# Performance work log

Measured on AMD Instinct MI355X. Metric: run time of the kernel, lower is better.

Reference implementation:

```python
import jax, jax.numpy as jnp
import numpy as np

T, B, D, H = 2048, 2, 1024, 16
NH, DH = H // 2, D // H   # 8 heads per direction, d_head = 64
DFF = 4096


def layer_norm(x, g, b, eps=1e-5):
    mu = jnp.mean(x, axis=-1, keepdims=True)
    var = jnp.mean(jnp.square(x - mu), axis=-1, keepdims=True)
    return (x - mu) * jax.lax.rsqrt(var + eps) * g + b


def rel_shift(x):
    # x: [q, k, b, n] -> Transformer-XL relative shift
    q, k, b, n = x.shape
    x = jnp.concatenate([jnp.zeros((q, 1, b, n), x.dtype), x], axis=1)
    return x.reshape(k + 1, q, b, n)[1:].reshape(q, k, b, n)


def rel_attn(w, r, mask, qkv_w, r_w, r_w_bias, r_r_bias):
    # w: [T, B, D], r: [R, 1, D], mask: [T, T] bool (True = masked)
    t, b, _ = w.shape
    heads = jnp.einsum('tbd,ed->tbe', w, qkv_w)              # [T,B,3*NH*DH]
    q, k, v = jnp.split(heads, 3, axis=-1)
    q = q.reshape(t, b, NH, DH)
    k = k.reshape(t, b, NH, DH)
    v = v.reshape(t, b, NH, DH)
    rk = jnp.einsum('rd,ed->re', r[:, 0, :], r_w).reshape(-1, NH, DH)  # [R,NH,DH]
    AC = jnp.einsum('ibnd,jbnd->ijbn', q + r_w_bias, k)
    BD = rel_shift(jnp.einsum('ibnd,jnd->ijbn', q + r_r_bias, rk))
    score = (AC + BD) * (1.0 / np.sqrt(DH))
    score = jnp.where(mask[:, :, None, None], jnp.finfo(score.dtype).min, score)
    prob = jax.nn.softmax(score, axis=1)
    vec = jnp.einsum('ijbn,jbnd->ibnd', prob, v)
    return vec.reshape(t, b, NH * DH)


def setup_inputs() -> dict:
    key = jax.random.key(0)
    ks = jax.random.split(key, 24)
    s = 0.02
    causal = jnp.triu(jnp.ones((T, T), dtype=bool), k=1)
    return {
        'x': jax.random.normal(ks[0], (T, B, D), jnp.float32),
        'pos': jax.random.normal(ks[1], (T, 1, D), jnp.float32),
        'mask_fwd': causal,
        'mask_bwd': causal,
        'ln1_g': jnp.ones((D,), jnp.float32), 'ln1_b': jnp.zeros((D,), jnp.float32),
        'ln2_g': jnp.ones((D,), jnp.float32), 'ln2_b': jnp.zeros((D,), jnp.float32),
        'ln3_g': jnp.ones((D,), jnp.float32), 'ln3_b': jnp.zeros((D,), jnp.float32),
        'qkv_f': jax.random.normal(ks[2], (3 * NH * DH, D), jnp.float32) * s,
        'rnet_f': jax.random.normal(ks[3], (NH * DH, D), jnp.float32) * s,
        'rwb_f': jax.random.normal(ks[4], (NH, DH), jnp.float32) * s,
        'rrb_f': jax.random.normal(ks[5], (NH, DH), jnp.float32) * s,
        'qkv_b': jax.random.normal(ks[6], (3 * NH * DH, D), jnp.float32) * s,
        'rnet_b': jax.random.normal(ks[7], (NH * DH, D), jnp.float32) * s,
        'rwb_b': jax.random.normal(ks[8], (NH, DH), jnp.float32) * s,
        'rrb_b': jax.random.normal(ks[9], (NH, DH), jnp.float32) * s,
        'wo': jax.random.normal(ks[10], (D, D), jnp.float32) * s,
        'bo': jnp.zeros((D,), jnp.float32),
        'w1': jax.random.normal(ks[11], (DFF, D), jnp.float32) * s,
        'b1': jnp.zeros((DFF,), jnp.float32),
        'w2': jax.random.normal(ks[12], (D, DFF), jnp.float32) * s,
        'b2': jnp.zeros((D,), jnp.float32),
    }


def reference(x, pos, mask_fwd, mask_bwd,
              ln1_g, ln1_b, ln2_g, ln2_b, ln3_g, ln3_b,
              qkv_f, rnet_f, rwb_f, rrb_f,
              qkv_b, rnet_b, rwb_b, rrb_b,
              wo, bo, w1, b1, w2, b2):
    # --- bidirectional relative attention ---
    q_fwd = layer_norm(x, ln1_g, ln1_b)
    q_bwd = layer_norm(jnp.flip(x, axis=0), ln2_g, ln2_b)
    out_fwd = rel_attn(q_fwd, pos, mask_fwd, qkv_f, rnet_f, rwb_f, rrb_f)
    out_bwd = rel_attn(q_bwd, pos, mask_bwd, qkv_b, rnet_b, rwb_b, rrb_b)
    out = jnp.concatenate([out_fwd, jnp.flip(out_bwd, axis=0)], axis=-1)
    out = jnp.einsum('tbd,ed->tbe', out, wo) + bo
    h = x + out                     # postprocess_attn: dropout(id) + residual
    # --- feed forward: LN -> Linear -> ReLU -> Linear -> residual ---
    y = layer_norm(h, ln3_g, ln3_b)
    y = jax.nn.relu(jnp.einsum('tbd,fd->tbf', y, w1) + b1)
    y = jnp.einsum('tbf,df->tbd', y, w2) + b2
    return h + y
```

## Files before the change

kernel.cpp:

```cpp
#include <hip/hip_runtime.h>
#include <cstdint>
#include <cstddef>


typedef unsigned short ushort_t;
typedef __bf16 bf16x8 __attribute__((ext_vector_type(8)));
typedef float f32x4 __attribute__((ext_vector_type(4)));
typedef unsigned short us8 __attribute__((ext_vector_type(8)));
typedef unsigned short us4 __attribute__((ext_vector_type(4)));

#define DEV static __device__ __forceinline__

DEV ushort_t f2bf(float x) {
  union { float f; unsigned u; } v; v.f = x;
  unsigned r = (v.u + 0x7FFFu + ((v.u >> 16) & 1u)) >> 16;
  return (ushort_t)r;
}
DEV ushort_t f2bt(float x) {
  union { float f; unsigned u; } v; v.f = x;
  return (ushort_t)(v.u >> 16);
}
DEV float bf2f(ushort_t h) {
  union { unsigned u; float f; } v; v.u = ((unsigned)h) << 16;
  return v.f;
}
DEV float fexp2(float x) { float r; asm("v_exp_f32 %0, %1" : "=v"(r) : "v"(x)); return r; }
DEV f32x4 mfma16(bf16x8 a, bf16x8 b, f32x4 c) {
  return __builtin_amdgcn_mfma_f32_16x16x32_bf16(a, b, c, 0, 0, 0);
}
DEV void gld16(const void* g, void* l) {
  __builtin_amdgcn_global_load_lds((const __attribute__((address_space(1))) void*)g,
                                   (__attribute__((address_space(3))) void*)l,
                                   16, 0, 0);
}

constexpr float SCLQ = 0.125f * 1.44269504088896f;

constexpr size_t O_QKV_F  = 0;
constexpr size_t O_QKV_B  = 3145728;
constexpr size_t O_RNET_F = 6291456;
constexpr size_t O_RNET_B = 7340032;
constexpr size_t O_WO     = 8388608;
constexpr size_t O_W1     = 10485760;
constexpr size_t O_W2     = 18874368;
constexpr size_t O_RKREV_F= 27262976;
constexpr size_t O_RKREV_B= 29360128;
constexpr size_t O_QAC_F  = 31457280;
constexpr size_t O_QBD_F  = 35651584;
constexpr size_t O_KK_F   = 39845888;
constexpr size_t O_VT_F   = 44040192;
constexpr size_t O_QAC_B  = 48234496;
constexpr size_t O_QBD_B  = 52428800;
constexpr size_t O_KK_B   = 56623104;
constexpr size_t O_VT_B   = 60817408;
constexpr size_t O_H      = 65011712;
constexpr size_t O_LN3    = 81788928;
constexpr size_t ZONE     = 90177536;
constexpr size_t O_POS    = ZONE + 0;
constexpr size_t O_LN1    = ZONE + 4194304;
constexpr size_t O_LN2    = ZONE + 12582912;
constexpr size_t O_HEADS_F= ZONE + 20971520;
constexpr size_t O_HEADS_B= ZONE + 33554432;
constexpr size_t O_ACAT   = ZONE + 0;
constexpr size_t O_FFNM   = ZONE + 8388608;

struct CvtArgs {
  const float* src[8];
  ushort_t* dst[8];
  int bstart[8];
};
__global__ __launch_bounds__(256)
void cvt_all_k(CvtArgs a) {
  int bx = blockIdx.x;
  int s = 0;
#pragma unroll
  for (int k = 1; k < 8; ++k) if (bx >= a.bstart[k]) s = k;
  int i = (bx - a.bstart[s]) * 256 + threadIdx.x;
  float4 v = reinterpret_cast<const float4*>(a.src[s])[i];
  us4 o; o[0] = f2bf(v.x); o[1] = f2bf(v.y); o[2] = f2bf(v.z); o[3] = f2bf(v.w);
  reinterpret_cast<us4*>(a.dst[s])[i] = o;
}

__global__ __launch_bounds__(256)
void ln_dual_k(const float* __restrict__ x,
               const float* __restrict__ g1, const float* __restrict__ b1,
               const float* __restrict__ g2, const float* __restrict__ b2,
               ushort_t* __restrict__ o1, ushort_t* __restrict__ o2) {
  __shared__ float sbuf[8];
  const int row = blockIdx.x;
  const int tid = threadIdx.x;
  const float* xr = x + (size_t)row * 1024;
  float4 v = reinterpret_cast<const float4*>(xr)[tid];
  float s  = v.x + v.y + v.z + v.w;
  float s2 = v.x*v.x + v.y*v.y + v.z*v.z + v.w*v.w;
  for (int m = 32; m >= 1; m >>= 1) { s += __shfl_xor(s, m, 64); s2 += __shfl_xor(s2, m, 64); }
  int w = tid >> 6;
  if ((tid & 63) == 0) { sbuf[w] = s; sbuf[4 + w] = s2; }
  __syncthreads();
  float S  = sbuf[0] + sbuf[1] + sbuf[2] + sbuf[3];
  float S2 = sbuf[4] + sbuf[5] + sbuf[6] + sbuf[7];
  float mu  = S * (1.f / 1024.f);
  float var = S2 * (1.f / 1024.f) - mu * mu;
  float inv = rsqrtf(var + 1e-5f);
  int t = row >> 1, b = row & 1;
  size_t r2 = ((size_t)(2047 - t) * 2 + b) * 1024;
  float4 G1 = reinterpret_cast<const float4*>(g1)[tid];
  float4 B1 = reinterpret_cast<const float4*>(b1)[tid];
  float4 G2 = reinterpret_cast<const float4*>(g2)[tid];
  float4 B2 = reinterpret_cast<const float4*>(b2)[tid];
  float n0 = (v.x - mu) * inv, n1 = (v.y - mu) * inv, n2 = (v.z - mu) * inv, n3 = (v.w - mu) * inv;
  us4 a, c;
  a[0] = f2bf(n0 * G1.x + B1.x); a[1] = f2bf(n1 * G1.y + B1.y);
  a[2] = f2bf(n2 * G1.z + B1.z); a[3] = f2bf(n3 * G1.w + B1.w);
  c[0] = f2bf(n0 * G2.x + B2.x); c[1] = f2bf(n1 * G2.y + B2.y);
  c[2] = f2bf(n2 * G2.z + B2.z); c[3] = f2bf(n3 * G2.w + B2.w);
  reinterpret_cast<us4*>(o1 + (size_t)row * 1024)[tid] = a;
  reinterpret_cast<us4*>(o2 + r2)[tid] = c;
}

__global__ __launch_bounds__(256)
void ln_one_k(const float* __restrict__ x,
              const float* __restrict__ g1, const float* __restrict__ b1,
              ushort_t* __restrict__ o1) {
  __shared__ float sbuf[8];
  const int row = blockIdx.x;
  const int tid = threadIdx.x;
  const float* xr = x + (size_t)row * 1024;
  float4 v = reinterpret_cast<const float4*>(xr)[tid];
  float s  = v.x + v.y + v.z + v.w;
  float s2 = v.x*v.x + v.y*v.y + v.z*v.z + v.w*v.w;
  for (int m = 32; m >= 1; m >>= 1) { s += __shfl_xor(s, m, 64); s2 += __shfl_xor(s2, m, 64); }
  int w = tid >> 6;
  if ((tid & 63) == 0) { sbuf[w] = s; sbuf[4 + w] = s2; }
  __syncthreads();
  float S  = sbuf[0] + sbuf[1] + sbuf[2] + sbuf[3];
  float S2 = sbuf[4] + sbuf[5] + sbuf[6] + sbuf[7];
  float mu  = S * (1.f / 1024.f);
  float var = S2 * (1.f / 1024.f) - mu * mu;
  float inv = rsqrtf(var + 1e-5f);
  float4 G1 = reinterpret_cast<const float4*>(g1)[tid];
  float4 B1 = reinterpret_cast<const float4*>(b1)[tid];
  us4 a;
  a[0] = f2bf((v.x - mu) * inv * G1.x + B1.x);
  a[1] = f2bf((v.y - mu) * inv * G1.y + B1.y);
  a[2] = f2bf((v.z - mu) * inv * G1.z + B1.z);
  a[3] = f2bf((v.w - mu) * inv * G1.w + B1.w);
  reinterpret_cast<us4*>(o1 + (size_t)row * 1024)[tid] = a;
}

template <int EPI>
__global__ __launch_bounds__(256)
void gemm_bt(const ushort_t* __restrict__ A, const ushort_t* __restrict__ B,
             void* __restrict__ C, const float* __restrict__ bias,
             const float* __restrict__ resid, int M, int N, int K) {
  __shared__ ushort_t As[128 * 64];
  __shared__ ushort_t Bs[128 * 64];
  const int tid = threadIdx.x;
  const int lane = tid & 63;
  const int w = tid >> 6;
  const int wm = w >> 1, wn = w & 1;
  const int row0 = blockIdx.y * 128, col0 = blockIdx.x * 128;
  const int lr = lane & 15;
  const int lkb = (lane >> 4) * 8;
  const int rr = lane >> 3;
  const int scb = ((lane & 7) ^ rr) * 8;
  const f32x4 fz = {0.f, 0.f, 0.f, 0.f};
  f32x4 acc[4][4];
#pragma unroll
  for (int i = 0; i < 4; ++i)
#pragma unroll
    for (int j = 0; j < 4; ++j) acc[i][j] = fz;

  for (int k0 = 0; k0 < K; k0 += 64) {
    __syncthreads();
#pragma unroll
    for (int it = 0; it < 4; ++it) {
      int rbase = it * 32 + w * 8;
      gld16(A + (size_t)(row0 + rbase + rr) * K + k0 + scb, (char*)As + rbase * 128);
      gld16(B + (size_t)(col0 + rbase + rr) * K + k0 + scb, (char*)Bs + rbase * 128);
    }
    __syncthreads();
#pragma unroll
    for (int kk = 0; kk < 64; kk += 32) {
      bf16x8 af[4], bfr[4];
#pragma unroll
      for (int mi = 0; mi < 4; ++mi) {
        int r = wm * 64 + mi * 16 + lr;
        int off = (r * 128 + (kk + lkb) * 2) ^ ((r & 7) << 4);
        af[mi] = *reinterpret_cast<const bf16x8*>((char*)As + off);
      }
#pragma unroll
      for (int ni = 0; ni < 4; ++ni) {
        int r = wn * 64 + ni * 16 + lr;
        int off = (r * 128 + (kk + lkb) * 2) ^ ((r & 7) << 4);
        bfr[ni] = *reinterpret_cast<const bf16x8*>((char*)Bs + off);
      }
#pragma unroll
      for (int mi = 0; mi < 4; ++mi)
#pragma unroll
        for (int ni = 0; ni < 4; ++ni)
          acc[mi][ni] = mfma16(af[mi], bfr[ni], acc[mi][ni]);
    }
  }
#pragma unroll
  for (int mi = 0; mi < 4; ++mi)
#pragma unroll
    for (int ni = 0; ni < 4; ++ni)
#pragma unroll
      for (int r = 0; r < 4; ++r) {
        int row = row0 + wm * 64 + mi * 16 + (lane >> 4) * 4 + r;
        int col = col0 + wn * 64 + ni * 16 + lr;
        float v = acc[mi][ni][r];
        if (EPI == 0) {
          ((ushort_t*)C)[(size_t)row * N + col] = f2bf(v);
        } else if (EPI == 1) {
          v += bias[col]; v = v > 0.f ? v : 0.f;
          ((ushort_t*)C)[(size_t)row * N + col] = f2bf(v);
        } else {
          v += bias[col] + resid[(size_t)row * N + col];
          ((float*)C)[(size_t)row * N + col] = v;
        }
      }
}

template <int EPI>
__global__ __launch_bounds__(256)
void gemm64(const ushort_t* __restrict__ A0, const ushort_t* __restrict__ A1,
            const ushort_t* __restrict__ B0, const ushort_t* __restrict__ B1,
            void* __restrict__ C0, void* __restrict__ C1,
            const float* __restrict__ bias, const float* __restrict__ resid,
            const float* __restrict__ rw0, const float* __restrict__ rr0,
            const float* __restrict__ rw1, const float* __restrict__ rr1,
            int M, int N, int K) {
  __shared__ ushort_t As[64 * 64];
  __shared__ ushort_t Bs[128 * 64];
  const ushort_t* A = blockIdx.z ? A1 : A0;
  const ushort_t* B = blockIdx.z ? B1 : B0;
  void* C = blockIdx.z ? (void*)C1 : (void*)C0;
  const int tid = threadIdx.x;
  const int lane = tid & 63;
  const int w = tid >> 6;
  const int wm = w >> 1, wn = w & 1;
  const int row0 = blockIdx.y * 64, col0 = blockIdx.x * 128;
  const int lr = lane & 15;
  const int lkb = (lane >> 4) * 8;
  const int rr = lane >> 3;
  const int scb = ((lane & 7) ^ rr) * 8;
  const f32x4 fz = {0.f, 0.f, 0.f, 0.f};
  f32x4 acc[2][4];
#pragma unroll
  for (int i = 0; i < 2; ++i)
#pragma unroll
    for (int j = 0; j < 4; ++j) acc[i][j] = fz;

  for (int k0 = 0; k0 < K; k0 += 64) {
    __syncthreads();
#pragma unroll
    for (int it = 0; it < 2; ++it) {
      int rbase = it * 32 + w * 8;
      gld16(A + (size_t)(row0 + rbase + rr) * K + k0 + scb, (char*)As + rbase * 128);
    }
#pragma unroll
    for (int it = 0; it < 4; ++it) {
      int rbase = it * 32 + w * 8;
      gld16(B + (size_t)(col0 + rbase + rr) * K + k0 + scb, (char*)Bs + rbase * 128);
    }
    __syncthreads();
#pragma unroll
    for (int kk = 0; kk < 64; kk += 32) {
      bf16x8 af[2], bfr[4];
#pragma unroll
      for (int mi = 0; mi < 2; ++mi) {
        int r = wm * 32 + mi * 16 + lr;
        int off = (r * 128 + (kk + lkb) * 2) ^ ((r & 7) << 4);
        af[mi] = *reinterpret_cast<const bf16x8*>((char*)As + off);
      }
#pragma unroll
      for (int ni = 0; ni < 4; ++ni) {
        int r = wn * 64 + ni * 16 + lr;
        int off = (r * 128 + (kk + lkb) * 2) ^ ((r & 7) << 4);
        bfr[ni] = *reinterpret_cast<const bf16x8*>((char*)Bs + off);
      }
#pragma unroll
      for (int mi = 0; mi < 2; ++mi)
#pragma unroll
        for (int ni = 0; ni < 4; ++ni)
          acc[mi][ni] = mfma16(af[mi], bfr[ni], acc[mi][ni]);
    }
  }
#pragma unroll
  for (int mi = 0; mi < 2; ++mi)
#pragma unroll
    for (int ni = 0; ni < 4; ++ni)
#pragma unroll
      for (int r = 0; r < 4; ++r) {
        int row = row0 + wm * 32 + mi * 16 + (lane >> 4) * 4 + r;
        int col = col0 + wn * 64 + ni * 16 + lr;
        float v = acc[mi][ni][r];
        if (EPI == 0) {
          ((ushort_t*)C)[(size_t)row * N + col] = f2bf(v);
        } else if (EPI == 1) {
          v += bias[col]; v = v > 0.f ? v : 0.f;
          ((ushort_t*)C)[(size_t)row * N + col] = f2bf(v);
        } else if (EPI == 2) {
          v += bias[col] + resid[(size_t)row * N + col];
          ((float*)C)[(size_t)row * N + col] = v;
        } else if (EPI == 3) {
          int nn = col >> 6, dh = col & 63;
          ((ushort_t*)C)[((size_t)nn * 2048 + (2047 - row)) * 64 + dh] = f2bf(v);
        } else {
          char* wsb = (char*)C;
          const int dirz = blockIdx.z;
          const float* rwb = dirz ? rw1 : rw0;
          const float* rrb = dirz ? rr1 : rr0;
          int t = row >> 1, bb = row & 1;
          if (col < 512) {
            int nn = col >> 6, dh = col & 63;
            ushort_t* q_ac = (ushort_t*)(wsb + (dirz ? O_QAC_B : O_QAC_F));
            ushort_t* q_bd = (ushort_t*)(wsb + (dirz ? O_QBD_B : O_QBD_F));
            size_t o = ((size_t)(bb * 8 + nn) * 2048 + t) * 64 + dh;
            q_ac[o] = f2bf((v + rwb[col]) * SCLQ);
            q_bd[o] = f2bf((v + rrb[col]) * SCLQ);
          } else if (col < 1024) {
            int cc = col - 512;
            int nn = cc >> 6, dh = cc & 63;
            ushort_t* kout = (ushort_t*)(wsb + (dirz ? O_KK_B : O_KK_F));
            kout[((size_t)(bb * 8 + nn) * 2048 + t) * 64 + dh] = f2bf(v);
          } else {
            ushort_t* hv = (ushort_t*)(wsb + (dirz ? O_HEADS_B : O_HEADS_F));
            hv[(size_t)row * 1536 + col] = f2bf(v);
          }
        }
      }
}

__global__ __launch_bounds__(256)
void v_trans2_k(const ushort_t* __restrict__ hf, const ushort_t* __restrict__ hb2,
                char* __restrict__ wsb) {
  __shared__ float tile[64][65];
  const int dir = blockIdx.z;
  const ushort_t* heads = dir ? hb2 : hf;
  ushort_t* vt = (ushort_t*)(wsb + (dir ? O_VT_B : O_VT_F));
  int tt0 = blockIdx.x * 64;
  int bn = blockIdx.y;
  int b = bn >> 3, n = bn & 7;
  int tid = threadIdx.x;
#pragma unroll
  for (int i = 0; i < 16; ++i) {
    int rr = i * 4 + (tid >> 6);
    int cc = tid & 63;
    tile[rr][cc] = bf2f(heads[(size_t)((tt0 + rr) * 2 + b) * 1536 + 1024 + n * 64 + cc]);
  }
  __syncthreads();
#pragma unroll
  for (int i = 0; i < 16; ++i) {
    int dh = i * 4 + (tid >> 6);
    int tt = tid & 63;
    vt[((size_t)bn * 64 + dh) * 2048 + tt0 + tt] = f2bf(tile[tt][dh]);
  }
}

__global__ __launch_bounds__(256)
void attn_k(const char* __restrict__ wsb, ushort_t* __restrict__ outp) {
  __shared__ ushort_t Kbuf[2][64 * 64];
  __shared__ ushort_t Vbuf[2][64 * 64];
  __shared__ alignas(16) ushort_t Gs[4][16 * 84];
  __shared__ ushort_t Ps[4][1024];

  const int tid = threadIdx.x;
  const int lane = tid & 63;
  const int w = tid >> 6;
  const int il = lane & 15;
  const int g = lane >> 4;
  const int lkb = g * 8;
  const int rr = lane >> 3;
  const int scb = ((lane & 7) ^ rr) * 8;

  const int id = (int)(blockIdx.x + (blockIdx.y << 4) + (blockIdx.z << 8));
  const int xcd = id & 7;
  const int ord = id >> 3;
  const int pair = xcd * 4 + (ord & 3);
  const int bx = ord >> 2;
  const int bn = pair & 15;
  const int dir = pair >> 4;

  const ushort_t* qac  = (const ushort_t*)(wsb + (dir ? O_QAC_B : O_QAC_F));
  const ushort_t* qbd  = (const ushort_t*)(wsb + (dir ? O_QBD_B : O_QBD_F));
  const ushort_t* kkv  = (const ushort_t*)(wsb + (dir ? O_KK_B  : O_KK_F));
  const ushort_t* vtp  = (const ushort_t*)(wsb + (dir ? O_VT_B  : O_VT_F));
  const ushort_t* rkrev= (const ushort_t*)(wsb + (dir ? O_RKREV_B : O_RKREV_F));
  const int colbase = dir ? 512 : 0;

  const size_t hb = (size_t)bn * 2048;
  const size_t vbase = (size_t)bn * 64;
  const size_t nb = (size_t)(bn & 7) * 2048;
  const int b = bn >> 3;
  const int n = bn & 7;

  ushort_t* gw = Gs[w];
  char* pw = (char*)Ps[w];

  for (int half = 0; half < 2; ++half) {
    const int it = half ? bx : (31 - bx);
    const int i0 = it * 64;
    const int NT = it + 1;
    const int iw0 = i0 + w * 16;

    auto STAGE = [&](int bi, int j0) {
      ushort_t* kb = Kbuf[bi] + w * 512;
      ushort_t* vbp = Vbuf[bi] + w * 512;
      gld16(kkv + (hb + j0 + w * 8 + rr) * 64 + scb, kb);
      gld16(kkv + (hb + j0 + 32 + w * 8 + rr) * 64 + scb, kb + 2048);
      gld16(vtp + (vbase + w * 8 + rr) * 2048 + j0 + scb, vbp);
      gld16(vtp + (vbase + 32 + w * 8 + rr) * 2048 + j0 + scb, vbp + 2048);
    };

    bf16x8 qa[2], qb[2];
#pragma unroll
    for (int kf = 0; kf < 2; ++kf) {
      size_t off = (hb + iw0 + il) * 64 + kf * 32 + lkb;
      qa[kf] = *reinterpret_cast<const bf16x8*>(qac + off);
      qb[kf] = *reinterpret_cast<const bf16x8*>(qbd + off);
    }

    const f32x4 fz = {0.f, 0.f, 0.f, 0.f};
    f32x4 Oa[4];
#pragma unroll
    for (int nf = 0; nf < 4; ++nf) Oa[nf] = fz;
    float lsum = 0.f;

    STAGE(0, 0);
    __syncthreads();
    int cur = 0;
    for (int jt = 0; jt < NT; ++jt) {
      const int j0 = jt * 64;

      bf16x8 bd0[5], bd1[5];
      const int dbase = iw0 - j0 - 63;
#pragma unroll
      for (int ng = 0; ng < 5; ++ng) {
        int d = dbase + ng * 16 + il;
        d = d < 0 ? 0 : (d > 2047 ? 2047 : d);
        const ushort_t* bp = rkrev + (nb + d) * 64 + lkb;
        bd0[ng] = *reinterpret_cast<const bf16x8*>(bp);
        bd1[ng] = *reinterpret_cast<const bf16x8*>(bp + 32);
      }
      if (jt + 1 < NT) STAGE(cur ^ 1, j0 + 64);

      const ushort_t* Ks = Kbuf[cur];
      const ushort_t* Vs = Vbuf[cur];
      f32x4 S[4], G[5];
#pragma unroll
      for (int nf = 0; nf < 4; ++nf) S[nf] = fz;
#pragma unroll
      for (int ng = 0; ng < 5; ++ng) G[ng] = fz;
      __builtin_amdgcn_s_setprio(1);
#pragma unroll
      for (int kf = 0; kf < 2; ++kf)
#pragma unroll
        for (int nf = 0; nf < 4; ++nf) {
          int r = nf * 16 + il;
          int off = (r * 128 + (kf * 32 + lkb) * 2) ^ ((r & 7) << 4);
          S[nf] = mfma16(*reinterpret_cast<const bf16x8*>((char*)Ks + off), qa[kf], S[nf]);
        }
#pragma unroll
      for (int ng = 0; ng < 5; ++ng) {
        G[ng] = mfma16(bd0[ng], qb[0], G[ng]);
        G[ng] = mfma16(bd1[ng], qb[1], G[ng]);
      }
      __builtin_amdgcn_s_setprio(0);
#pragma unroll
      for (int ng = 0; ng < 5; ++ng) {
        us4 pk;
        pk[0] = f2bt(G[ng][0]); pk[1] = f2bt(G[ng][1]);
        pk[2] = f2bt(G[ng][2]); pk[3] = f2bt(G[ng][3]);
        *reinterpret_cast<us4*>(gw + il * 84 + ng * 16 + g * 4) = pk;
      }
      asm volatile("s_waitcnt lgkmcnt(0)" ::: "memory");
      const bool full = (j0 + 63 <= iw0);
#pragma unroll
      for (int nf = 0; nf < 4; ++nf) {
        int c3 = il - (nf * 16 + g * 4 + 3) + 63;
        int base4 = c3 & ~3;
        int o = c3 & 3;
        const ushort_t* gp = gw + il * 84 + base4;
        uint64_t av = *reinterpret_cast<const uint64_t*>(gp);
        uint64_t bv2 = *reinterpret_cast<const uint64_t*>(gp + 4);
        uint64_t vv = o ? ((av >> (16 * o)) | (bv2 << (64 - 16 * o))) : av;
#pragma unroll
        for (int r = 0; r < 4; ++r) {
          int jl = nf * 16 + g * 4 + r;
          float sv = S[nf][r] + bf2f((ushort_t)(vv >> (16 * (3 - r))));
          if (!full) sv = (j0 + jl <= iw0 + il) ? sv : -1e30f;
          S[nf][r] = sv;
        }
      }
#pragma unroll
      for (int nf = 0; nf < 4; ++nf) {
        us4 pk;
#pragma unroll
        for (int r = 0; r < 4; ++r) {
          float p = fexp2(S[nf][r]);
          lsum += p;
          pk[r] = f2bt(p);
        }
        int off = (il * 128 + (nf * 16 + g * 4) * 2) ^ ((il & 7) << 4);
        *reinterpret_cast<us4*>(pw + off) = pk;
      }
      asm volatile("s_waitcnt lgkmcnt(0)" ::: "memory");
      __builtin_amdgcn_s_setprio(1);
#pragma unroll
      for (int kf = 0; kf < 2; ++kf) {
        int poff = (il * 128 + (kf * 32 + lkb) * 2) ^ ((il & 7) << 4);
        bf16x8 pt = *reinterpret_cast<const bf16x8*>(pw + poff);
#pragma unroll
        for (int nf = 0; nf < 4; ++nf) {
          int r = nf * 16 + il;
          int voff = (r * 128 + (kf * 32 + lkb) * 2) ^ ((r & 7) << 4);
          Oa[nf] = mfma16(*reinterpret_cast<const bf16x8*>((char*)Vs + voff), pt, Oa[nf]);
        }
      }
      __builtin_amdgcn_s_setprio(0);
      __syncthreads();
      cur ^= 1;
    }
    lsum += __shfl_xor(lsum, 16, 64);
    lsum += __shfl_xor(lsum, 32, 64);
    float invl = 1.f / lsum;
    int ig = iw0 + il;
    int tout = dir ? (2047 - ig) : ig;
    size_t orow = ((size_t)tout * 2 + b) * 1024 + colbase + n * 64;
#pragma unroll
    for (int nf = 0; nf < 4; ++nf) {
      us4 pk;
#pragma unroll
      for (int r = 0; r < 4; ++r) pk[r] = f2bf(Oa[nf][r] * invl);
      *reinterpret_cast<us4*>(outp + orow + nf * 16 + g * 4) = pk;
    }
  }
}

extern "C" void kernel_launch(void* const* d_in, const int* in_sizes, int n_in,
                              void* d_out, int out_size, void* d_ws, size_t ws_size,
                              hipStream_t stream) {
  (void)in_sizes; (void)n_in; (void)out_size; (void)ws_size;
  const float* x    = (const float*)d_in[0];
  const float* pos  = (const float*)d_in[1];
  const float* ln1g = (const float*)d_in[4];
  const float* ln1b = (const float*)d_in[5];
  const float* ln2g = (const float*)d_in[6];
  const float* ln2b = (const float*)d_in[7];
  const float* ln3g = (const float*)d_in[8];
  const float* ln3b = (const float*)d_in[9];
  const float* qkvf = (const float*)d_in[10];
  const float* rnetf= (const float*)d_in[11];
  const float* rwbf = (const float*)d_in[12];
  const float* rrbf = (const float*)d_in[13];
  const float* qkvb = (const float*)d_in[14];
  const float* rnetb= (const float*)d_in[15];
  const float* rwbb = (const float*)d_in[16];
  const float* rrbb = (const float*)d_in[17];
  const float* wo   = (const float*)d_in[18];
  const float* bo   = (const float*)d_in[19];
  const float* w1   = (const float*)d_in[20];
  const float* b1   = (const float*)d_in[21];
  const float* w2   = (const float*)d_in[22];
  const float* b2   = (const float*)d_in[23];
  float* out = (float*)d_out;
  char* ws = (char*)d_ws;
  auto U = [&](size_t off) { return (ushort_t*)(ws + off); };

  CvtArgs ca;
  const float* srcs[8] = {qkvf, qkvb, rnetf, rnetb, wo, w1, w2, pos};
  size_t dsts[8] = {O_QKV_F, O_QKV_B, O_RNET_F, O_RNET_B, O_WO, O_W1, O_W2, O_POS};
  int bl[8] = {1536, 1536, 512, 512, 1024, 4096, 4096, 2048};
  int cum = 0;
  for (int s = 0; s < 8; ++s) {
    ca.src[s] = srcs[s];
    ca.dst[s] = U(dsts[s]);
    ca.bstart[s] = cum;
    cum += bl[s];
  }
  cvt_all_k<<<dim3(cum), dim3(256), 0, stream>>>(ca);

  ln_dual_k<<<dim3(4096), dim3(256), 0, stream>>>(x, ln1g, ln1b, ln2g, ln2b, U(O_LN1), U(O_LN2));

  gemm64<4><<<dim3(12, 64, 2), dim3(256), 0, stream>>>(
      U(O_LN1), U(O_LN2), U(O_QKV_F), U(O_QKV_B), ws, ws,
      nullptr, nullptr, rwbf, rrbf, rwbb, rrbb, 4096, 1536, 1024);
  gemm64<3><<<dim3(4, 32, 2), dim3(256), 0, stream>>>(
      U(O_POS), U(O_POS), U(O_RNET_F), U(O_RNET_B), U(O_RKREV_F), U(O_RKREV_B),
      nullptr, nullptr, nullptr, nullptr, nullptr, nullptr, 2048, 512, 1024);

  v_trans2_k<<<dim3(32, 16, 2), dim3(256), 0, stream>>>(U(O_HEADS_F), U(O_HEADS_B), ws);

  attn_k<<<dim3(16, 16, 2), dim3(256), 0, stream>>>(ws, U(O_ACAT));

  gemm64<2><<<dim3(8, 64, 1), dim3(256), 0, stream>>>(
      U(O_ACAT), U(O_ACAT), U(O_WO), U(O_WO), ws + O_H, ws + O_H,
      bo, x, nullptr, nullptr, nullptr, nullptr, 4096, 1024, 1024);

  ln_one_k<<<dim3(4096), dim3(256), 0, stream>>>((const float*)(ws + O_H), ln3g, ln3b, U(O_LN3));
  gemm_bt<1><<<dim3(32, 32), dim3(256), 0, stream>>>(U(O_LN3), U(O_W1), U(O_FFNM), b1, nullptr, 4096, 4096, 1024);
  gemm64<2><<<dim3(8, 64, 1), dim3(256), 0, stream>>>(
      U(O_FFNM), U(O_FFNM), U(O_W2), U(O_W2), out, out,
      b2, (const float*)(ws + O_H), nullptr, nullptr, nullptr, nullptr, 4096, 1024, 4096);
}
```

Measured before the change: 335.6 us.

## Use 128x128 tiles for QKV GEMM and split-K FFN2 with reduction kernel

Adds a 128x128-tile GEMM variant with separate leading dimensions and uses it for the QKV projection, halving the number of row blocks. The second FFN GEMM is split along K into two halves via blockIdx.z, each writing fp32 partials. A new elementwise kernel then sums the partials with bias and residual. The aim is more data reuse per block and more parallelism for the long-K GEMM, at the cost of extra partial-buffer traffic and one more launch.

After: 329.0 us. Within noise of the previous version (-2.0%).

```diff
diff --git a/kernel.cpp b/kernel.cpp
--- a/kernel.cpp
+++ b/kernel.cpp
@@ -63,6 +63,7 @@
 constexpr size_t O_HEADS_B= ZONE + 33554432;
 constexpr size_t O_ACAT   = ZONE + 0;
 constexpr size_t O_FFNM   = ZONE + 8388608;
+constexpr size_t O_FPART  = O_QAC_F;
 
 struct CvtArgs {
   const float* src[8];
@@ -225,14 +226,13 @@
 
 template <int EPI>
 __global__ __launch_bounds__(256)
-void gemm64(const ushort_t* __restrict__ A0, const ushort_t* __restrict__ A1,
-            const ushort_t* __restrict__ B0, const ushort_t* __restrict__ B1,
-            void* __restrict__ C0, void* __restrict__ C1,
-            const float* __restrict__ bias, const float* __restrict__ resid,
-            const float* __restrict__ rw0, const float* __restrict__ rr0,
-            const float* __restrict__ rw1, const float* __restrict__ rr1,
-            int M, int N, int K) {
-  __shared__ ushort_t As[64 * 64];
+void gemm_bt2(const ushort_t* __restrict__ A0, const ushort_t* __restrict__ A1,
+              const ushort_t* __restrict__ B0, const ushort_t* __restrict__ B1,
+              void* __restrict__ C0, void* __restrict__ C1,
+              const float* __restrict__ rw0, const float* __restrict__ rr0,
+              const float* __restrict__ rw1, const float* __restrict__ rr1,
+              int M, int N, int K, int lda, int ldb) {
+  __shared__ ushort_t As[128 * 64];
   __shared__ ushort_t Bs[128 * 64];
   const ushort_t* A = blockIdx.z ? A1 : A0;
   const ushort_t* B = blockIdx.z ? B1 : B0;
@@ -241,37 +241,33 @@
   const int lane = tid & 63;
   const int w = tid >> 6;
   const int wm = w >> 1, wn = w & 1;
-  const int row0 = blockIdx.y * 64, col0 = blockIdx.x * 128;
+  const int row0 = blockIdx.y * 128, col0 = blockIdx.x * 128;
   const int lr = lane & 15;
   const int lkb = (lane >> 4) * 8;
   const int rr = lane >> 3;
   const int scb = ((lane & 7) ^ rr) * 8;
   const f32x4 fz = {0.f, 0.f, 0.f, 0.f};
-  f32x4 acc[2][4];
-#pragma unroll
-  for (int i = 0; i < 2; ++i)
+  f32x4 acc[4][4];
+#pragma unroll
+  for (int i = 0; i < 4; ++i)
 #pragma unroll
     for (int j = 0; j < 4; ++j) acc[i][j] = fz;
 
   for (int k0 = 0; k0 < K; k0 += 64) {
     __syncthreads();
 #pragma unroll
-    for (int it = 0; it < 2; ++it) {
-      int rbase = it * 32 + w * 8;
-      gld16(A + (size_t)(row0 + rbase + rr) * K + k0 + scb, (char*)As + rbase * 128);
-    }
-#pragma unroll
     for (int it = 0; it < 4; ++it) {
       int rbase = it * 32 + w * 8;
-      gld16(B + (size_t)(col0 + rbase + rr) * K + k0 + scb, (char*)Bs + rbase * 128);
+      gld16(A + (size_t)(row0 + rbase + rr) * lda + k0 + scb, (char*)As + rbase * 128);
+      gld16(B + (size_t)(col0 + rbase + rr) * ldb + k0 + scb, (char*)Bs + rbase * 128);
     }
     __syncthreads();
 #pragma unroll
     for (int kk = 0; kk < 64; kk += 32) {
-      bf16x8 af[2], bfr[4];
-#pragma unroll
-      for (int mi = 0; mi < 2; ++mi) {
-        int r = wm * 32 + mi * 16 + lr;
+      bf16x8 af[4], bfr[4];
+#pragma unroll
+      for (int mi = 0; mi < 4; ++mi) {
+        int r = wm * 64 + mi * 16 + lr;
         int off = (r * 128 + (kk + lkb) * 2) ^ ((r & 7) << 4);
         af[mi] = *reinterpret_cast<const bf16x8*>((char*)As + off);
       }
@@ -282,33 +278,26 @@
         bfr[ni] = *reinterpret_cast<const bf16x8*>((char*)Bs + off);
       }
 #pragma unroll
-      for (int mi = 0; mi < 2; ++mi)
+      for (int mi = 0; mi < 4; ++mi)
 #pragma unroll
         for (int ni = 0; ni < 4; ++ni)
           acc[mi][ni] = mfma16(af[mi], bfr[ni], acc[mi][ni]);
     }
   }
 #pragma unroll
-  for (int mi = 0; mi < 2; ++mi)
+  for (int mi = 0; mi < 4; ++mi)
 #pragma unroll
     for (int ni = 0; ni < 4; ++ni)
 #pragma unroll
       for (int r = 0; r < 4; ++r) {
-        int row = row0 + wm * 32 + mi * 16 + (lane >> 4) * 4 + r;
+        int row = row0 + wm * 64 + mi * 16 + (lane >> 4) * 4 + r;
         int col = col0 + wn * 64 + ni * 16 + lr;
         float v = acc[mi][ni][r];
         if (EPI == 0) {
           ((ushort_t*)C)[(size_t)row * N + col] = f2bf(v);
-        } else if (EPI == 1) {
-          v += bias[col]; v = v > 0.f ? v : 0.f;
-          ((ushort_t*)C)[(size_t)row * N + col] = f2bf(v);
-        } else if (EPI == 2) {
-          v += bias[col] + resid[(size_t)row * N + col];
+        } else if (EPI == 5) {
           ((float*)C)[(size_t)row * N + col] = v;
-        } else if (EPI == 3) {
-          int nn = col >> 6, dh = col & 63;
-          ((ushort_t*)C)[((size_t)nn * 2048 + (2047 - row)) * 64 + dh] = f2bf(v);
-        } else {
+        } else if (EPI == 4) {
           char* wsb = (char*)C;
           const int dirz = blockIdx.z;
           const float* rwb = dirz ? rw1 : rw0;
@@ -332,6 +321,107 @@
           }
         }
       }
+}
+
+template <int EPI>
+__global__ __launch_bounds__(256)
+void gemm64(const ushort_t* __restrict__ A0, const ushort_t* __restrict__ A1,
+            const ushort_t* __restrict__ B0, const ushort_t* __restrict__ B1,
+            void* __restrict__ C0, void* __restrict__ C1,
+            const float* __restrict__ bias, const float* __restrict__ resid,
+            int M, int N, int K) {
+  __shared__ ushort_t As[64 * 64];
+  __shared__ ushort_t Bs[128 * 64];
+  const ushort_t* A = blockIdx.z ? A1 : A0;
+  const ushort_t* B = blockIdx.z ? B1 : B0;
+  void* C = blockIdx.z ? (void*)C1 : (void*)C0;
+  const int tid = threadIdx.x;
+  const int lane = tid & 63;
+  const int w = tid >> 6;
+  const int wm = w >> 1, wn = w & 1;
+  const int row0 = blockIdx.y * 64, col0 = blockIdx.x * 128;
+  const int lr = lane & 15;
+  const int lkb = (lane >> 4) * 8;
+  const int rr = lane >> 3;
+  const int scb = ((lane & 7) ^ rr) * 8;
+  const f32x4 fz = {0.f, 0.f, 0.f, 0.f};
+  f32x4 acc[2][4];
+#pragma unroll
+  for (int i = 0; i < 2; ++i)
+#pragma unroll
+    for (int j = 0; j < 4; ++j) acc[i][j] = fz;
+
+  for (int k0 = 0; k0 < K; k0 += 64) {
+    __syncthreads();
+#pragma unroll
+    for (int it = 0; it < 2; ++it) {
+      int rbase = it * 32 + w * 8;
+      gld16(A + (size_t)(row0 + rbase + rr) * K + k0 + scb, (char*)As + rbase * 128);
+    }
+#pragma unroll
+    for (int it = 0; it < 4; ++it) {
+      int rbase = it * 32 + w * 8;
+      gld16(B + (size_t)(col0 + rbase + rr) * K + k0 + scb, (char*)Bs + rbase * 128);
+    }
+    __syncthreads();
+#pragma unroll
+    for (int kk = 0; kk < 64; kk += 32) {
+      bf16x8 af[2], bfr[4];
+#pragma unroll
+      for (int mi = 0; mi < 2; ++mi) {
+        int r = wm * 32 + mi * 16 + lr;
+        int off = (r * 128 + (kk + lkb) * 2) ^ ((r & 7) << 4);
+        af[mi] = *reinterpret_cast<const bf16x8*>((char*)As + off);
+      }
+#pragma unroll
+      for (int ni = 0; ni < 4; ++ni) {
+        int r = wn * 64 + ni * 16 + lr;
+        int off = (r * 128 + (kk + lkb) * 2) ^ ((r & 7) << 4);
+        bfr[ni] = *reinterpret_cast<const bf16x8*>((char*)Bs + off);
+      }
+#pragma unroll
+      for (int mi = 0; mi < 2; ++mi)
+#pragma unroll
+        for (int ni = 0; ni < 4; ++ni)
+          acc[mi][ni] = mfma16(af[mi], bfr[ni], acc[mi][ni]);
+    }
+  }
+#pragma unroll
+  for (int mi = 0; mi < 2; ++mi)
+#pragma unroll
+    for (int ni = 0; ni < 4; ++ni)
+#pragma unroll
+      for (int r = 0; r < 4; ++r) {
+        int row = row0 + wm * 32 + mi * 16 + (lane >> 4) * 4 + r;
+        int col = col0 + wn * 64 + ni * 16 + lr;
+        float v = acc[mi][ni][r];
+        if (EPI == 2) {
+          v += bias[col] + resid[(size_t)row * N + col];
+          ((float*)C)[(size_t)row * N + col] = v;
+        } else if (EPI == 3) {
+          int nn = col >> 6, dh = col & 63;
+          ((ushort_t*)C)[((size_t)nn * 2048 + (2047 - row)) * 64 + dh] = f2bf(v);
+        }
+      }
+}
+
+__global__ __launch_bounds__(256)
+void ffn2_red_k(const float* __restrict__ p0, const float* __restrict__ p1,
+                const float* __restrict__ b2, const float* __restrict__ h,
+                float* __restrict__ out) {
+  const int row = blockIdx.x;
+  const int tid = threadIdx.x;
+  const size_t base = (size_t)row * 1024;
+  float4 a = reinterpret_cast<const float4*>(p0 + base)[tid];
+  float4 b = reinterpret_cast<const float4*>(p1 + base)[tid];
+  float4 hv = reinterpret_cast<const float4*>(h + base)[tid];
+  float4 bb = reinterpret_cast<const float4*>(b2)[tid];
+  float4 o;
+  o.x = a.x + b.x + hv.x + bb.x;
+  o.y = a.y + b.y + hv.y + bb.y;
+  o.z = a.z + b.z + hv.z + bb.z;
+  o.w = a.w + b.w + hv.w + bb.w;
+  reinterpret_cast<float4*>(out + base)[tid] = o;
 }
 
 __global__ __launch_bounds__(256)
@@ -585,12 +675,12 @@
 
   ln_dual_k<<<dim3(4096), dim3(256), 0, stream>>>(x, ln1g, ln1b, ln2g, ln2b, U(O_LN1), U(O_LN2));
 
-  gemm64<4><<<dim3(12, 64, 2), dim3(256), 0, stream>>>(
+  gemm_bt2<4><<<dim3(12, 32, 2), dim3(256), 0, stream>>>(
       U(O_LN1), U(O_LN2), U(O_QKV_F), U(O_QKV_B), ws, ws,
-      nullptr, nullptr, rwbf, rrbf, rwbb, rrbb, 4096, 1536, 1024);
+      rwbf, rrbf, rwbb, rrbb, 4096, 1536, 1024, 1024, 1024);
   gemm64<3><<<dim3(4, 32, 2), dim3(256), 0, stream>>>(
       U(O_POS), U(O_POS), U(O_RNET_F), U(O_RNET_B), U(O_RKREV_F), U(O_RKREV_B),
-      nullptr, nullptr, nullptr, nullptr, nullptr, nullptr, 2048, 512, 1024);
+      nullptr, nullptr, 2048, 512, 1024);
 
   v_trans2_k<<<dim3(32, 16, 2), dim3(256), 0, stream>>>(U(O_HEADS_F), U(O_HEADS_B), ws);
 
@@ -598,11 +688,16 @@
 
   gemm64<2><<<dim3(8, 64, 1), dim3(256), 0, stream>>>(
       U(O_ACAT), U(O_ACAT), U(O_WO), U(O_WO), ws + O_H, ws + O_H,
-      bo, x, nullptr, nullptr, nullptr, nullptr, 4096, 1024, 1024);
+      bo, x, 4096, 1024, 1024);
 
   ln_one_k<<<dim3(4096), dim3(256), 0, stream>>>((const float*)(ws + O_H), ln3g, ln3b, U(O_LN3));
   gemm_bt<1><<<dim3(32, 32), dim3(256), 0, stream>>>(U(O_LN3), U(O_W1), U(O_FFNM), b1, nullptr, 4096, 4096, 1024);
-  gemm64<2><<<dim3(8, 64, 1), dim3(256), 0, stream>>>(
-      U(O_FFNM), U(O_FFNM), U(O_W2), U(O_W2), out, out,
-      b2, (const float*)(ws + O_H), nullptr, nullptr, nullptr, nullptr, 4096, 1024, 4096);
-}
+
+  float* part0 = (float*)(ws + O_FPART);
+  float* part1 = part0 + (size_t)4096 * 1024;
+  gemm_bt2<5><<<dim3(8, 32, 2), dim3(256), 0, stream>>>(
+      U(O_FFNM), U(O_FFNM) + 2048, U(O_W2), U(O_W2) + 2048, part0, part1,
+      nullptr, nullptr, nullptr, nullptr, 4096, 1024, 2048, 4096, 4096);
+  ffn2_red_k<<<dim3(4096), dim3(256), 0, stream>>>(
+      part0, part1, b2, (const float*)(ws + O_H), out);
+}
```
